# Optimization experiments

Measured on AMD Instinct MI355X. Metric: run time of the kernel, lower is better.

Reference implementation:

```python
import jax, jax.numpy as jnp
import numpy as np


def _tridiag_solve(x, d, l, u):
    # Build dense tridiagonal M (faithful to the torch module) and solve.
    # x: [B, N, F]; d: [F]; l, u: [F-1]
    diag = jax.nn.softplus(d) + 2.0
    M = jnp.diag(diag) + jnp.diag(jnp.tanh(l), -1) + jnp.diag(jnp.tanh(u), 1)
    # solve M @ Y = x^T  -> Y: [B, F, N], then transpose back
    y = jnp.linalg.solve(M, jnp.swapaxes(x, -2, -1))
    return jnp.swapaxes(y, -2, -1)


def setup_inputs() -> dict:
    key = jax.random.key(0)
    ks = jax.random.split(key, 11)
    B, N = 8, 4096
    IN, HID, OUT = 512, 2048, 512
    s = 0.02
    return {
        "x": jax.random.normal(ks[0], (B, N, IN), dtype=jnp.float32),
        "d1": jax.random.normal(ks[1], (IN,), dtype=jnp.float32) * s,
        "l1": jax.random.normal(ks[2], (IN - 1,), dtype=jnp.float32) * s,
        "u1": jax.random.normal(ks[3], (IN - 1,), dtype=jnp.float32) * s,
        "W1": jax.random.normal(ks[4], (HID, IN), dtype=jnp.float32) * s,
        "b1": jax.random.normal(ks[5], (HID,), dtype=jnp.float32) * s,
        "d2": jax.random.normal(ks[6], (HID,), dtype=jnp.float32) * s,
        "l2": jax.random.normal(ks[7], (HID - 1,), dtype=jnp.float32) * s,
        "u2": jax.random.normal(ks[8], (HID - 1,), dtype=jnp.float32) * s,
        "W2": jax.random.normal(ks[9], (OUT, HID), dtype=jnp.float32) * s,
        "b2": jax.random.normal(ks[10], (OUT,), dtype=jnp.float32) * s,
    }


def reference(x, d1, l1, u1, W1, b1, d2, l2, u2, W2, b2):
    h = _tridiag_solve(x, d1, l1, u1)
    h = jax.nn.relu(jnp.einsum("bnf,hf->bnh", h, W1) + b1)
    h = _tridiag_solve(h, d2, l2, u2)
    out = jnp.einsum("bnh,oh->bno", h, W2) + b2
    return out
```

## Files before the change

### kernel.cpp

```cpp
#include <hip/hip_runtime.h>
#include <cstdint>

#define R_ROWS 32768
#define F1 512
#define F2 2048
#define NOUT 512

typedef __bf16 bf16x8 __attribute__((ext_vector_type(8)));
typedef float f32x4 __attribute__((ext_vector_type(4)));

__device__ __forceinline__ float bf2f(uint16_t b) {
  union { uint32_t u; float f; } v; v.u = ((uint32_t)b) << 16; return v.f;
}
__device__ __forceinline__ uint16_t f2bf(float f) {
  union { float f; uint32_t u; } v; v.f = f;
  uint32_t u = v.u;
  return (uint16_t)((u + 0x7fffu + ((u >> 16) & 1u)) >> 16);
}

union U4 { uint4 v; uint16_t s[8]; };

__global__ void sniff_kernel(const uint16_t* x, int* flag) {
  if (threadIdx.x == 0) {
    int bad = 0;
    for (int i = 0; i < 64; ++i) {
      uint32_t e = (x[i] >> 7) & 0xFFu;
      if (e != 0u && (e < 90u || e > 141u)) bad++;
    }
    *flag = (bad >= 8) ? 1 : 0;
  }
}

__global__ void conv_xb(const float* x, const float* b1, const float* b2,
                        uint16_t* xb, uint16_t* b1b, uint16_t* b2b,
                        const int* flag) {
  if (*flag != 1) return;
  const int NX = R_ROWS * F1 / 4;
  int q = blockIdx.x * blockDim.x + threadIdx.x;
  const float* src; uint16_t* dst; int base;
  if (q < NX)                        { src = x;  dst = xb;  base = q; }
  else if (q < NX + F2 / 4)          { src = b1; dst = b1b; base = q - NX; }
  else if (q < NX + F2/4 + NOUT/4)   { src = b2; dst = b2b; base = q - NX - F2/4; }
  else return;
  float4 v = ((const float4*)src)[base];
  ushort4 o;
  o.x = f2bf(v.x); o.y = f2bf(v.y); o.z = f2bf(v.z); o.w = f2bf(v.w);
  ((ushort4*)dst)[base] = o;
}

__launch_bounds__(256)
__global__ void prep_fused(const void* d1, const void* l1, const void* u1,
                           const void* d2, const void* l2, const void* u2,
                           float* f1, float* f2, const int* flag) {
  const bool inf32 = (*flag == 1);
  const int F = blockIdx.x ? F2 : F1;
  float* base = blockIdx.x ? f2 : f1;
  const void* dp = blockIdx.x ? d2 : d1;
  const void* lp = blockIdx.x ? l2 : l1;
  const void* up = blockIdx.x ? u2 : u1;

  __shared__ float sdiag[F2], stl[F2], stu[F2], sfw[F2], sib[F2];

  for (int i = threadIdx.x; i < F; i += 256) {
    float dv = inf32 ? ((const float*)dp)[i] : bf2f(((const uint16_t*)dp)[i]);
    sdiag[i] = log1pf(expf(dv)) + 2.0f;
    bool in = i < F - 1;
    float lv = in ? (inf32 ? ((const float*)lp)[i] : bf2f(((const uint16_t*)lp)[i])) : 0.0f;
    float uv = in ? (inf32 ? ((const float*)up)[i] : bf2f(((const uint16_t*)up)[i])) : 0.0f;
    stl[i] = in ? tanhf(lv) : 0.0f;
    stu[i] = in ? tanhf(uv) : 0.0f;
  }
  __syncthreads();
  if (threadIdx.x == 0) {
    float ib = __builtin_amdgcn_rcpf(sdiag[0]);
    sfw[0] = 0.0f; sib[0] = ib;
    #pragma unroll 8
    for (int i = 1; i < F; ++i) {
      float w = stu[i - 1] * ib;
      float b = fmaf(-w, stl[i - 1], sdiag[i]);
      ib = __builtin_amdgcn_rcpf(b);
      sfw[i] = w; sib[i] = ib;
    }
  }
  __syncthreads();
  for (int i = threadIdx.x; i < F; i += 256) {
    base[3 * F + i] = sfw[i];
    base[4 * F + i] = sib[i];
    base[5 * F + i] = stl[i] * sib[i];
  }
}

template<int F>
__launch_bounds__(256)
__global__ void solve_fused(const void* X, uint16_t* Y, const float* fact,
                            const int* flag, int allow_f32) {
  const bool inf32 = allow_f32 && (*flag == 1);
  constexpr int LPR = F / 32;
  constexpr int FP = F + (F >> 5);
  __shared__ float sfw[FP], sib[FP], sbk[FP];
  __shared__ uint4 sout[1024];
  for (int i = threadIdx.x; i < F; i += 256) {
    int ii = i + (i >> 5);
    sfw[ii] = fact[3 * F + i];
    sib[ii] = fact[4 * F + i];
    sbk[ii] = fact[5 * F + i];
  }
  __syncthreads();
  const int tid = threadIdx.x;
  int gt  = blockIdx.x * 256 + tid;
  int row = gt / LPR;
  int j   = gt % LPR;
  int k0  = j * 32;
  const size_t rb = (size_t)row * F;

  float xc[32];
  if (inf32) {
    const float* xr = (const float*)X + rb + k0;
    #pragma unroll
    for (int t = 0; t < 8; ++t) {
      float4 v = ((const float4*)xr)[t];
      xc[4*t] = v.x; xc[4*t+1] = v.y; xc[4*t+2] = v.z; xc[4*t+3] = v.w;
    }
  } else {
    const uint16_t* xr = (const uint16_t*)X + rb + k0;
    #pragma unroll
    for (int t = 0; t < 4; ++t) {
      U4 in; in.v = ((const uint4*)xr)[t];
      #pragma unroll
      for (int s = 0; s < 8; ++s) xc[8*t+s] = bf2f(in.s[s]);
    }
  }

  float dp = 0.0f;
  if (j > 0) {
    float xw[16];
    if (inf32) {
      const float* xr = (const float*)X + rb + k0 - 16;
      #pragma unroll
      for (int t = 0; t < 4; ++t) {
        float4 v = ((const float4*)xr)[t];
        xw[4*t] = v.x; xw[4*t+1] = v.y; xw[4*t+2] = v.z; xw[4*t+3] = v.w;
      }
    } else {
      const uint16_t* xr = (const uint16_t*)X + rb + k0 - 16;
      #pragma unroll
      for (int t = 0; t < 2; ++t) {
        U4 in; in.v = ((const uint4*)xr)[t];
        #pragma unroll
        for (int s = 0; s < 8; ++s) xw[8*t+s] = bf2f(in.s[s]);
      }
    }
    #pragma unroll
    for (int t = 0; t < 16; ++t) {
      int k = k0 - 16 + t;
      dp = fmaf(-sfw[k + (k >> 5)], dp, xw[t]);
    }
  }
  float dpv[32];
  #pragma unroll
  for (int t = 0; t < 32; ++t) {
    int k = k0 + t;
    dp = fmaf(-sfw[k + (k >> 5)], dp, xc[t]);
    dpv[t] = dp;
  }

  float wdp[16];
  #pragma unroll
  for (int t = 0; t < 16; ++t) wdp[t] = __shfl_down(dpv[t], 1);
  float yn = 0.0f;
  if (j < LPR - 1) {
    #pragma unroll
    for (int t = 15; t >= 0; --t) {
      int k = k0 + 32 + t;
      int kk = k + (k >> 5);
      yn = fmaf(-sbk[kk], yn, wdp[t] * sib[kk]);
    }
  }
  U4 out[4];
  #pragma unroll
  for (int t = 31; t >= 0; --t) {
    int k = k0 + t;
    int kk = k + (k >> 5);
    yn = fmaf(-sbk[kk], yn, dpv[t] * sib[kk]);
    out[t >> 3].s[t & 7] = f2bf(yn);
  }
  #pragma unroll
  for (int t = 0; t < 4; ++t) sout[tid * 4 + t] = out[t].v;
  __syncthreads();
  uint4* yg = (uint4*)Y + (size_t)blockIdx.x * 1024;
  #pragma unroll
  for (int i = 0; i < 4; ++i) yg[i * 256 + tid] = sout[i * 256 + tid];
}

__device__ __forceinline__ void gl_lds16(const uint16_t* g, uint16_t* l) {
  __builtin_amdgcn_global_load_lds((const __attribute__((address_space(1))) void*)g,
                                   (__attribute__((address_space(3))) void*)l, 16, 0, 0);
}

#define LOFF(bb, ab, h) ((bb) * 32768 + (ab) * 16384 + (h) * 8192)

#define GSTG(gp, bb, ab, h, kt) do {                                              \
    gl_lds16((gp) + (size_t)(h) * 128 * K + (kt),        lds + LOFF(bb, ab, h) + w * 512);        \
    gl_lds16((gp) + ((size_t)(h) * 128 + 64) * K + (kt), lds + LOFF(bb, ab, h) + 4096 + w * 512); \
  } while (0)

#define RD_A(mq) do {                                                             \
    _Pragma("unroll")                                                             \
    for (int fi = 0; fi < 4; ++fi) {                                              \
      af[fi][0] = *(const bf16x8*)(lds + curA + (mq) * 8192 + arow + fi * 1024 + c0); \
      af[fi][1] = *(const bf16x8*)(lds + curA + (mq) * 8192 + arow + fi * 1024 + c1); \
    }                                                                             \
  } while (0)

#define RD_B(nq) do {                                                             \
    _Pragma("unroll")                                                             \
    for (int fj = 0; fj < 2; ++fj) {                                              \
      bfr[nq][fj][0] = *(const bf16x8*)(lds + curB + (nq) * 8192 + brow + fj * 1024 + c0); \
      bfr[nq][fj][1] = *(const bf16x8*)(lds + curB + (nq) * 8192 + brow + fj * 1024 + c1); \
    }                                                                             \
  } while (0)

#define MMA_QUAD(mq, nq) do {                                                     \
    _Pragma("unroll")                                                             \
    for (int fi = 0; fi < 4; ++fi) {                                              \
      _Pragma("unroll")                                                           \
      for (int fj = 0; fj < 2; ++fj) {                                            \
        acc[(mq)*4+fi][(nq)*2+fj] = __builtin_amdgcn_mfma_f32_16x16x32_bf16(      \
            af[fi][0], bfr[nq][fj][0], acc[(mq)*4+fi][(nq)*2+fj], 0, 0, 0);       \
        acc[(mq)*4+fi][(nq)*2+fj] = __builtin_amdgcn_mfma_f32_16x16x32_bf16(      \
            af[fi][1], bfr[nq][fj][1], acc[(mq)*4+fi][(nq)*2+fj], 0, 0, 0);       \
      }                                                                           \
    }                                                                             \
  } while (0)

#define VMC(n) asm volatile("s_waitcnt vmcnt(" #n ")" ::: "memory")
#define BAR()  __builtin_amdgcn_s_barrier()
#define LGK0() do { asm volatile("s_waitcnt lgkmcnt(0)" ::: "memory");            \
                    __builtin_amdgcn_sched_barrier(0); } while (0)

template<bool RELU, bool FINAL, int NTN>
__launch_bounds__(512, 2)
__global__ void gemm8(const uint16_t* __restrict__ Aa, const uint16_t* __restrict__ Ab,
                      const uint16_t* __restrict__ Bw,
                      const uint16_t* __restrict__ bias0, const uint16_t* __restrict__ bias1,
                      void* __restrict__ Cout, int Nn, int K, const int* flag) {
  __shared__ __align__(16) uint16_t lds[65536];
  const int f = *flag;
  const uint16_t* A    = f ? Ab : Aa;
  const uint16_t* bias = f ? bias1 : bias0;

  const int tid = threadIdx.x;
  const int w = tid >> 6;
  const int l = tid & 63;
  const int wm = w >> 2;
  const int wn = w & 3;

  const int b = blockIdx.x;
  const int x = b & 7;
  const int g = b >> 3;
  const int nb = g & (NTN - 1);
  const int mb = (g / NTN) * 8 + x;
  const int MB = mb * 256, NB = nb * 256;
  const int NT = K >> 6;

  const int srow = w * 8 + (l >> 3);
  const int sch  = (l & 7) ^ ((l >> 3) & 7);
  const uint16_t* ag = A  + (size_t)(MB + srow) * K + sch * 8;
  const uint16_t* bg = Bw + (size_t)(NB + srow) * K + sch * 8;

  const int c0 = (((l >> 4) ^ (l & 7)) << 3);
  const int c1 = c0 ^ 32;
  const int arow = (wm * 64 + (l & 15)) * 64;
  const int brow = (wn * 32 + (l & 15)) * 64;

  f32x4 acc[8][4] = {};
  bf16x8 af[4][2];
  bf16x8 bfr[2][2][2];

  GSTG(ag, 0, 0, 0, 0);
  GSTG(bg, 0, 1, 0, 0);
  GSTG(bg, 0, 1, 1, 0);
  GSTG(ag, 0, 0, 1, 0);
  VMC(4);
  BAR();

  for (int t = 0; t < NT - 1; ++t) {
    const int cur  = t & 1;
    const int nxt  = cur ^ 1;
    const int curA = cur * 32768;
    const int curB = curA + 16384;
    const int kn   = (t + 1) * 64;
    RD_A(0); RD_B(0);
    GSTG(ag, nxt, 0, 0, kn);
    VMC(4); BAR(); LGK0();
    __builtin_amdgcn_s_setprio(1); MMA_QUAD(0, 0); __builtin_amdgcn_s_setprio(0);
    BAR();
    RD_B(1);
    GSTG(bg, nxt, 1, 0, kn);
    VMC(4); BAR(); LGK0();
    __builtin_amdgcn_s_setprio(1); MMA_QUAD(0, 1); __builtin_amdgcn_s_setprio(0);
    BAR();
    RD_A(1);
    GSTG(bg, nxt, 1, 1, kn);
    BAR(); LGK0();
    __builtin_amdgcn_s_setprio(1); MMA_QUAD(1, 0); __builtin_amdgcn_s_setprio(0);
    BAR();
    GSTG(ag, nxt, 0, 1, kn);
    VMC(4); BAR();
    __builtin_amdgcn_s_setprio(1); MMA_QUAD(1, 1); __builtin_amdgcn_s_setprio(0);
    BAR();
  }

  {
    const int curA = ((NT - 1) & 1) * 32768;
    const int curB = curA + 16384;
    RD_A(0); RD_B(0);
    __builtin_amdgcn_s_setprio(1); MMA_QUAD(0, 0); __builtin_amdgcn_s_setprio(0);
    VMC(2); BAR();
    RD_B(1);
    __builtin_amdgcn_s_setprio(1); MMA_QUAD(0, 1); __builtin_amdgcn_s_setprio(0);
    VMC(0); BAR();
    RD_A(1);
    MMA_QUAD(1, 0);
    MMA_QUAD(1, 1);
  }

  const bool outf32 = FINAL && (f != 0);
  const int ccol  = l & 15;
  const int crow4 = (l >> 4) * 4;
  #pragma unroll
  for (int j = 0; j < 4; ++j) {
    int gcol = NB + (j >> 1) * 128 + wn * 32 + (j & 1) * 16 + ccol;
    float bv = bf2f(bias[gcol]);
    #pragma unroll
    for (int i = 0; i < 8; ++i) {
      int grow = MB + (i >> 2) * 128 + wm * 64 + (i & 3) * 16 + crow4;
      #pragma unroll
      for (int rr = 0; rr < 4; ++rr) {
        float v = acc[i][j][rr] + bv;
        if (RELU) v = fmaxf(v, 0.0f);
        size_t idx = (size_t)(grow + rr) * Nn + gcol;
        if (outf32) ((float*)Cout)[idx]    = v;
        else        ((uint16_t*)Cout)[idx] = f2bf(v);
      }
    }
  }
}

extern "C" void kernel_launch(void* const* d_in, const int* in_sizes, int n_in,
                              void* d_out, int out_size, void* d_ws, size_t ws_size,
                              hipStream_t stream) {
  const void* x  = d_in[0];
  const void* d1 = d_in[1];
  const void* l1 = d_in[2];
  const void* u1 = d_in[3];
  const void* W1 = d_in[4];
  const void* b1 = d_in[5];
  const void* d2 = d_in[6];
  const void* l2 = d_in[7];
  const void* u2 = d_in[8];
  const void* W2 = d_in[9];
  const void* b2 = d_in[10];

  char* ws = (char*)d_ws;
  int*      flag = (int*)ws;
  float*    f1   = (float*)(ws + 256);
  float*    f2   = (float*)(ws + (64 << 10));
  uint16_t* b1b  = (uint16_t*)(ws + (128 << 10));
  uint16_t* b2b  = (uint16_t*)(ws + (136 << 10));
  uint16_t* W1s  = (uint16_t*)(ws + (1 << 20));
  uint16_t* W2s  = (uint16_t*)(ws + (3 << 20));
  uint16_t* xb   = (uint16_t*)(ws + ((size_t)8 << 20));
  uint16_t* H1   = (uint16_t*)(ws + ((size_t)40 << 20));

  sniff_kernel<<<1, 64, 0, stream>>>((const uint16_t*)x, flag);

  prep_fused<<<2, 256, 0, stream>>>(d1, l1, u1, d2, l2, u2, f1, f2, flag);

  solve_fused<F1><<<128, 256, 0, stream>>>(W1, W1s, f1, flag, 1);
  solve_fused<F2><<<128, 256, 0, stream>>>(W2, W2s, f2, flag, 1);

  {
    int quads = R_ROWS * F1 / 4 + F2 / 4 + NOUT / 4;
    conv_xb<<<(quads + 255) / 256, 256, 0, stream>>>(
        (const float*)x, (const float*)b1, (const float*)b2, xb, b1b, b2b, flag);
  }

  gemm8<true, false, 8><<<1024, 512, 0, stream>>>(
      (const uint16_t*)x, xb, W1s, (const uint16_t*)b1, b1b, H1, F2, F1, flag);

  gemm8<false, true, 2><<<256, 512, 0, stream>>>(
      H1, H1, W2s, (const uint16_t*)b2, b2b, d_out, NOUT, F2, flag);
}
```

Baseline: 382.5 us.

## Parallelize tridiagonal LU factor recurrence with warm-started per-thread chunks

Replaces the single-thread serial Thomas factorization in the prep kernel with per-thread chunks. Each thread restarts the pivot recurrence 16 steps before its chunk and relies on the strongly diagonally dominant matrix to make the effect of the starting guess negligible. This removes a serial loop of up to 2048 dependent steps, but the result is approximate and is only accurate because the diagonal dominance (softplus+2 against tanh of small values) makes the recurrence forget its start quickly.

```diff
diff --git a/kernel.cpp b/kernel.cpp
--- a/kernel.cpp
+++ b/kernel.cpp
@@ -59,7 +59,7 @@
   const void* lp = blockIdx.x ? l2 : l1;
   const void* up = blockIdx.x ? u2 : u1;
 
-  __shared__ float sdiag[F2], stl[F2], stu[F2], sfw[F2], sib[F2];
+  __shared__ float sdiag[F2], stl[F2], stu[F2];
 
   for (int i = threadIdx.x; i < F; i += 256) {
     float dv = inf32 ? ((const float*)dp)[i] : bf2f(((const uint16_t*)dp)[i]);
@@ -71,22 +71,28 @@
     stu[i] = in ? tanhf(uv) : 0.0f;
   }
   __syncthreads();
-  if (threadIdx.x == 0) {
-    float ib = __builtin_amdgcn_rcpf(sdiag[0]);
-    sfw[0] = 0.0f; sib[0] = ib;
-    #pragma unroll 8
-    for (int i = 1; i < F; ++i) {
-      float w = stu[i - 1] * ib;
-      float b = fmaf(-w, stl[i - 1], sdiag[i]);
-      ib = __builtin_amdgcn_rcpf(b);
-      sfw[i] = w; sib[i] = ib;
-    }
-  }
-  __syncthreads();
-  for (int i = threadIdx.x; i < F; i += 256) {
-    base[3 * F + i] = sfw[i];
-    base[4 * F + i] = sib[i];
-    base[5 * F + i] = stl[i] * sib[i];
+
+  const int t  = threadIdx.x;
+  const int CH = F >> 8;
+  const int s0 = t * CH;
+  const int j0 = (s0 >= 16) ? (s0 - 16) : 0;
+  float b  = sdiag[j0];
+  float ib = __builtin_amdgcn_rcpf(b);
+  for (int j = j0 + 1; j < s0; ++j) {
+    b  = fmaf(-stu[j - 1] * stl[j - 1], ib, sdiag[j]);
+    ib = __builtin_amdgcn_rcpf(b);
+  }
+  #pragma unroll
+  for (int q = 0; q < 8; ++q) {
+    if (q >= CH) break;
+    int i = s0 + q;
+    float w, nb;
+    if (i == 0) { w = 0.0f; nb = sdiag[0]; }
+    else        { w = stu[i - 1] * ib; nb = fmaf(-w, stl[i - 1], sdiag[i]); }
+    ib = __builtin_amdgcn_rcpf(nb);
+    base[3 * F + i] = w;
+    base[4 * F + i] = ib;
+    base[5 * F + i] = stl[i] * ib;
   }
 }
 
```

Result: faster. 319.2 us (-16.6%).
